# Optimization experiments

Hardware: AMD Instinct MI355X
Metric: run time of the kernel (lower is better)

The kernel has to match this reference:

```python
import jax, jax.numpy as jnp
import numpy as np

RMIN, RMAX = 10, 20
GAP = RMAX - RMIN          # 10
NUMR = GAP + 1             # 11
NSTEP = 64
BATCH = 8192
P = 128
HID = 64
MC = 10000
T_TOTAL = 1.0
DT = T_TOTAL / NSTEP
DXC = 0.5                  # D (x diffusion)
DYC = 0.5                  # Dy
RDOM = 5.0                 # reflecting sphere radius for xb
CAP_EPS = 0.1              # capture distance
F32 = jnp.float32


def _jump_size(uvals, ridx, jump_measure):
    # uvals: [M] uniforms, ridx: [M] int row index into [NUMR, 2*GAP] measure
    cnt = (uvals[:, None] < jump_measure[ridx]).sum(axis=1)
    ind = 2 * GAP - cnt
    return jnp.where(ind < GAP, ind + 1, -(ind - GAP + 1)).astype(jnp.int32)


def _forward(u, jump_r, jump_l, W1, b1, W2, b2, W3, b3, emb,
             Wf1, bf1, Wf2, bf2, Wf3, bf3,
             rt0, xt0, yt0, dBxt, dByt, jump_unif, size_unif, mc_unif,
             jump_measure, cr, cfr):
    fix_x = jnp.array([1.0, 0.0, 0.0], F32)
    G = jnp.array([[0.0, 0.0], [0.0, 1.0], [-1.0, 0.0]], F32)  # grad_eucl_polar

    # Monte-Carlo jump compensation: E[jump_l(jump_size(r))] * cr, per r level
    ridx_mc = jnp.tile(jnp.arange(NUMR, dtype=jnp.int32), MC)
    s = _jump_size(mc_unif, ridx_mc, jump_measure)
    a = jnp.abs(s) - 1
    mcj = jump_l[0][a] * (s > 0)[:, None] + jump_l[1][a] * (s < 0)[:, None]
    mc_jump = mcj.reshape(MC, NUMR, P).mean(axis=0) * cr  # [NUMR, P]

    eye = jnp.broadcast_to(jnp.eye(3, dtype=F32), (BATCH, 3, 3))
    carry0 = (rt0, xt0, xt0, yt0, eye, eye,
              jnp.ones((BATCH, 1), F32) * u,        # u_pre
              jnp.zeros((BATCH, 1), F32),           # fun
              jnp.ones((BATCH, 1), F32))            # run mask

    def reflect(pos, gt):
        nr = jnp.linalg.norm(pos, axis=1, keepdims=True)
        nb = pos / jnp.maximum(nr, 1e-12)
        out = nr[:, 0] > RDOM
        pos = jnp.where(out[:, None], nb * (2.0 * RDOM - nr), pos)
        proj = jnp.einsum('bi,bij->bj', nb, gt)
        gt = jnp.where(out[:, None, None], gt - 2.0 * nb[:, :, None] * proj[:, None, :], gt)
        return pos, gt

    def step(carry, xs):
        rt, xt, xt_in, yt_in, gtx, gty, u_pre, fun, run = carry
        dbx, dby, ju, su, w1, bb1, w2, bb2, w3, bb3, em, wf1, bff1, wf2, bff2, wf3, bff3 = xs
        ridx = jnp.clip(rt - RMIN, 0, GAP)
        jump_on = ju < cr[ridx, 0] * DT
        drt = _jump_size(su, ridx, jump_measure) * jump_on.astype(jnp.int32)
        # polar angles of xt (theta shifted by pi/2, as in forward)
        nx = jnp.maximum(jnp.linalg.norm(xt, axis=1), 1e-12)
        th = jnp.arccos(jnp.clip(xt[:, 2] / nx, -1.0, 1.0)) - jnp.pi / 2
        ph = jnp.arctan2(xt[:, 1], xt[:, 0])
        ct, st_, cp, sp = jnp.cos(th), jnp.sin(th), jnp.cos(ph), jnp.sin(ph)
        z = jnp.zeros_like(ct)
        # T_inv = Rz(phi) @ Ry(theta - pi/2), maps local frame at fix_x to xt
        T_inv = jnp.stack([jnp.stack([cp * ct, -sp, cp * st_], 1),
                           jnp.stack([sp * ct, cp, sp * st_], 1),
                           jnp.stack([-st_, z, ct], 1)], axis=1)  # [B,3,3]
        inp6 = jnp.concatenate([xt_in, yt_in], axis=1)  # [B,6]
        # TNN: low-rank net, r-embedding contracted with MLP output [B,P,6]
        h = jnp.tanh(inp6 @ w1 + bb1)
        h = jnp.tanh(h @ w2 + bb2)
        gu = jnp.einsum('bp,bpo->bo', em[ridx], (h @ w3 + bb3).reshape(BATCH, P, 6))
        v = jnp.einsum('bi,bij->bj', gu[:, :3], gtx)
        v = jnp.einsum('bi,bij->bj', v, T_inv)
        grad_ux = v @ G                                     # [B,2]
        grad_uy = jnp.einsum('bi,bij->bj', gu[:, 3:], gty)  # [B,3]
        aidx = jnp.clip(jnp.abs(drt) - 1, 0, GAP - 1)
        jl = jump_l[0][aidx] * (drt > 0)[:, None] + jump_l[1][aidx] * (drt < 0)[:, None]
        hf = jnp.tanh(inp6 @ wf1 + bff1)
        hf = jnp.tanh(hf @ wf2 + bff2)
        jx = hf @ wf3 + bff3                                 # FNN [B,P]
        jump = (jx * jump_r[ridx] * (jl - mc_jump[ridx] * DT)).sum(1, keepdims=True)
        rtf = rt.astype(F32)[:, None]
        sdx = jnp.sqrt(2.0 * DXC) / rtf
        diff = (sdx * (grad_ux * dbx).sum(1, keepdims=True)
                + jnp.sqrt(2.0 * DYC) * (grad_uy * dby).sum(1, keepdims=True) + jump)
        u_pre = u_pre + run * jnp.exp(-fun) * diff
        fun = fun + cfr[ridx] * DT
        # SDE update on the sphere (local angular increment rotated by T_inv)
        dX = sdx * dbx
        tht = dX[:, 0] + jnp.pi / 2
        pht = dX[:, 1]
        cart = jnp.stack([jnp.sin(tht) * jnp.cos(pht),
                          jnp.sin(tht) * jnp.sin(pht),
                          jnp.cos(tht)], 1) - fix_x
        dX3 = jnp.einsum('bij,bj->bi', T_inv, cart)
        xt = xt + dX3
        xt_in = xt_in + jnp.einsum('bij,bj->bi', gtx, dX3)
        yt_in = yt_in + jnp.sqrt(2.0 * DYC) * jnp.einsum('bij,bj->bi', gty, dby)
        rt = jnp.clip(rt + drt, RMIN, RMAX)
        xt_in, gtx = reflect(xt_in, gtx)
        yt_in, gty = reflect(yt_in, gty)
        cap = jnp.linalg.norm(xt_in - yt_in, axis=1, keepdims=True) < CAP_EPS
        run = run * jnp.where(cap, 0.0, 1.0)
        return (rt, xt, xt_in, yt_in, gtx, gty, u_pre, fun, run), None

    xs = (dBxt, dByt, jump_unif, size_unif, W1, b1, W2, b2, W3, b3, emb,
          Wf1, bf1, Wf2, bf2, Wf3, bf3)
    carry, _ = jax.lax.scan(step, carry0, xs)
    rt, xt, xt_in, yt_in, gtx, gty, u_pre, fun, run = carry
    u0v = jnp.exp(-jnp.sum((xt_in - yt_in) ** 2, axis=1, keepdims=True))
    u_rel = run * u0v * jnp.exp(-fun)
    return u_pre, u_rel


def setup_inputs() -> dict:
    key = jax.random.key(0)
    ks = jax.random.split(key, 24)

    def nrm(k, shape, fan):
        return jax.random.normal(k, shape, dtype=F32) / np.float32(np.sqrt(fan))

    # birth/death rate tables, forward equation: alpha(r,k)=mu(r+k,k), beta(r,k)=lamb(r-k,k)
    kk = np.arange(1, GAP + 1, dtype=np.float32)
    rr = np.arange(RMIN, RMAX + 1, dtype=np.float32)[:, None]
    lamb = 0.6 * rr / (kk * (kk + 1))
    mu = 0.5 * rr / (kk * (kk + 1))
    alpha = 0.5 * (rr + kk) / (kk * (kk + 1))
    beta = 0.6 * np.maximum(rr - kk, 0.0) / (kk * (kk + 1))
    jm = np.concatenate([alpha, beta], axis=1).cumsum(axis=1)
    cr = jm[:, -1:]
    jump_measure = jm / cr
    cfr = lamb.sum(1, keepdims=True) + mu.sum(1, keepdims=True) - cr

    x0 = jax.random.normal(ks[17], (BATCH, 3), dtype=F32)
    x0 = x0 / jnp.linalg.norm(x0, axis=1, keepdims=True)
    y0 = jax.random.normal(ks[18], (BATCH, 3), dtype=F32)

    return dict(
        u=jax.random.uniform(ks[0], (1,), dtype=F32),
        jump_r=nrm(ks[1], (NUMR, P), P),
        jump_l=nrm(ks[2], (2, GAP, P), P),
        W1=nrm(ks[3], (NSTEP, 6, HID), 6), b1=jnp.zeros((NSTEP, HID), F32),
        W2=nrm(ks[4], (NSTEP, HID, HID), HID), b2=jnp.zeros((NSTEP, HID), F32),
        W3=nrm(ks[5], (NSTEP, HID, P * 6), HID), b3=jnp.zeros((NSTEP, P * 6), F32),
        emb=nrm(ks[6], (NSTEP, NUMR, P), P),
        Wf1=nrm(ks[7], (NSTEP, 6, HID), 6), bf1=jnp.zeros((NSTEP, HID), F32),
        Wf2=nrm(ks[8], (NSTEP, HID, HID), HID), bf2=jnp.zeros((NSTEP, HID), F32),
        Wf3=nrm(ks[9], (NSTEP, HID, P), HID), bf3=jnp.zeros((NSTEP, P), F32),
        rt0=jax.random.randint(ks[10], (BATCH,), RMIN, RMAX + 1, dtype=jnp.int32),
        xt0=x0,
        yt0=y0,
        dBxt=jax.random.normal(ks[11], (NSTEP, BATCH, 2), dtype=F32) * np.float32(np.sqrt(DT)),
        dByt=jax.random.normal(ks[12], (NSTEP, BATCH, 3), dtype=F32) * np.float32(np.sqrt(DT)),
        jump_unif=jax.random.uniform(ks[13], (NSTEP, BATCH), dtype=F32),
        size_unif=jax.random.uniform(ks[14], (NSTEP, BATCH), dtype=F32),
        mc_unif=jax.random.uniform(ks[15], (MC * NUMR,), dtype=F32),
        jump_measure=jnp.asarray(jump_measure),
        cr=jnp.asarray(cr),
        cfr=jnp.asarray(cfr),
    )


def reference(u, jump_r, jump_l, W1, b1, W2, b2, W3, b3, emb,
              Wf1, bf1, Wf2, bf2, Wf3, bf3,
              rt0, xt0, yt0, dBxt, dByt, jump_unif, size_unif, mc_unif,
              jump_measure, cr, cfr):
    return _forward(u, jump_r, jump_l, W1, b1, W2, b2, W3, b3, emb,
                    Wf1, bf1, Wf2, bf2, Wf3, bf3,
                    rt0, xt0, yt0, dBxt, dByt, jump_unif, size_unif, mc_unif,
                    jump_measure, cr, cfr)
```

## Files before the change

kernel.cpp:

```cpp
#include <hip/hip_runtime.h>
#include <math.h>

#define NUMR 11
#define NSTEP 64
#define BATCH 8192
#define PDIM 128
#define MC 10000
#define DT (1.0f/64.0f)
#define RDOM 5.0f
#define CAP_EPS 0.1f
#define TP (NSTEP*BATCH)

#define OFF_HIST 0
#define OFF_W3EB 256
#define OFF_B3E  180480
#define OFF_BT   186112
#define OFF_BB   1087232
#define OFF_W2A  1101312
#define OFF_WF2A 1232384
#define OFF_GEO  1363456
#define OFF_SM   7654912
#define OFF_CONTRIB 8703488

typedef __attribute__((ext_vector_type(8))) short short8;
typedef __attribute__((ext_vector_type(4))) float f32x4;

__device__ __forceinline__ float tanh_f(float x) {
    float e = __expf(2.0f * x);
    return 1.0f - 2.0f * __builtin_amdgcn_rcpf(e + 1.0f);
}
__device__ __forceinline__ unsigned short bf16bits(float f) {
    unsigned u = __float_as_uint(f);
    return (unsigned short)((u + 0x7FFFu + ((u >> 16) & 1u)) >> 16);
}
__device__ __forceinline__ float bf16f(unsigned short s) {
    return __uint_as_float(((unsigned)s) << 16);
}
__device__ __forceinline__ unsigned cvt_pk_bf16(float lo, float hi) {
    unsigned r;
    asm("v_cvt_pk_bf16_f32 %0, %1, %2" : "=v"(r) : "v"(lo), "v"(hi));
    return r;
}

__device__ __forceinline__ void reflect3(float* p, float* g) {
    float nr = sqrtf(p[0]*p[0] + p[1]*p[1] + p[2]*p[2]);
    if (nr > RDOM) {
        float inv = 1.0f / fmaxf(nr, 1e-12f);
        float nb0 = p[0]*inv, nb1 = p[1]*inv, nb2 = p[2]*inv;
        float sc = 2.0f*RDOM - nr;
        p[0] = nb0*sc; p[1] = nb1*sc; p[2] = nb2*sc;
        #pragma unroll
        for (int j = 0; j < 3; ++j) {
            float proj = nb0*g[j] + nb1*g[3+j] + nb2*g[6+j];
            g[j]   -= 2.0f*nb0*proj;
            g[3+j] -= 2.0f*nb1*proj;
            g[6+j] -= 2.0f*nb2*proj;
        }
    }
}

__launch_bounds__(256)
__global__ void k_prep(const int* __restrict__ rt0, const float* __restrict__ xt0,
                       const float* __restrict__ yt0, const float* __restrict__ dBx,
                       const float* __restrict__ dBy, const float* __restrict__ junif,
                       const float* __restrict__ sunif, const float* __restrict__ jm,
                       const float* __restrict__ cr, const float* __restrict__ cfr,
                       const float* __restrict__ mcu,
                       const float* __restrict__ W2, const float* __restrict__ Wf2,
                       const float* __restrict__ W3, const float* __restrict__ b3,
                       const float* __restrict__ emb, const float* __restrict__ Wf3,
                       const float* __restrict__ bf3, const float* __restrict__ jump_r,
                       const float* __restrict__ jump_l,
                       float* ws, int* hist, float* out) {
    __shared__ float smem[6440];
    int blk = blockIdx.x, tid = threadIdx.x;

    if (blk < 128) {
        float* sjm = smem; float* scr = smem + 220; float* smul = smem + 231;
        for (int i = tid; i < 220; i += 256) sjm[i] = jm[i];
        if (tid < 11) { scr[tid] = cr[tid]; smul[tid] = __expf(-cfr[tid]*DT); }
        __syncthreads();
        if (tid >= 64) return;
        int p = blk * 64 + tid;

        int rt = rt0[p];
        float xt[3], xin[3], yin[3], gtx[9], gty[9];
        #pragma unroll
        for (int i = 0; i < 3; ++i) { xt[i] = xt0[p*3+i]; xin[i] = xt[i]; yin[i] = yt0[p*3+i]; }
        #pragma unroll
        for (int i = 0; i < 9; ++i) { gtx[i] = (i % 4 == 0) ? 1.f : 0.f; gty[i] = gtx[i]; }
        float ef = 1.f, run = 1.f;

        float ju = junif[p], su = sunif[p];
        float dbx0 = dBx[(size_t)p*2], dbx1 = dBx[(size_t)p*2+1];
        float dby0 = dBy[(size_t)p*3], dby1 = dBy[(size_t)p*3+1], dby2 = dBy[(size_t)p*3+2];

        float* GEO = ws + OFF_GEO;
        float* SM  = ws + OFF_SM;
        #pragma unroll 1
        for (int t = 0; t < NSTEP; ++t) {
            float nju=0.f,nsu=0.f,ndbx0=0.f,ndbx1=0.f,ndby0=0.f,ndby1=0.f,ndby2=0.f;
            if (t < NSTEP-1) {
                int nb = (t+1)*BATCH + p;
                nju = junif[nb]; nsu = sunif[nb];
                ndbx0 = dBx[(size_t)nb*2]; ndbx1 = dBx[(size_t)nb*2+1];
                ndby0 = dBy[(size_t)nb*3]; ndby1 = dBy[(size_t)nb*3+1]; ndby2 = dBy[(size_t)nb*3+2];
            }
            int base = t*BATCH + p;
            int r = rt - 10;
            int jon = (ju < scr[r]*DT) ? 1 : 0;
            int cnt = 0;
            #pragma unroll
            for (int j = 0; j < 20; ++j) cnt += (su < sjm[r*20+j]) ? 1 : 0;
            int ind = 20 - cnt;
            int drt = (ind < 10) ? (ind+1) : -(ind-9);
            drt = jon ? drt : 0;
            int sa = (drt > 0) ? (drt-1) : ((drt < 0) ? (9-drt) : 0);
            int jf = (drt != 0) ? 1 : 0;

            float nx = fmaxf(sqrtf(xt[0]*xt[0]+xt[1]*xt[1]+xt[2]*xt[2]), 1e-12f);
            float c = fminf(1.f, fmaxf(-1.f, xt[2]/nx));
            float ct = sqrtf(fmaxf(0.f, 1.f - c*c));
            float st = -c;
            float rxy2 = xt[0]*xt[0] + xt[1]*xt[1];
            float cp = 1.f, sp = 0.f;
            if (rxy2 > 0.f) { float ir = 1.0f/sqrtf(rxy2); cp = xt[0]*ir; sp = xt[1]*ir; }
            float Ti[9];
            Ti[0]=cp*ct; Ti[1]=-sp; Ti[2]=cp*st;
            Ti[3]=sp*ct; Ti[4]=cp;  Ti[5]=sp*st;
            Ti[6]=-st;   Ti[7]=0.f; Ti[8]=ct;

            float sdx = 1.0f/(float)(r+10);
            float scale = run * ef;

            float cx[3], cy[3];
            #pragma unroll
            for (int i = 0; i < 3; ++i) {
                float w31 = gtx[i*3]*Ti[1] + gtx[i*3+1]*Ti[4] + gtx[i*3+2]*Ti[7];
                float w32 = gtx[i*3]*Ti[2] + gtx[i*3+1]*Ti[5] + gtx[i*3+2]*Ti[8];
                cx[i] = sdx * (w31*dbx1 - w32*dbx0);
                cy[i] = gty[i*3]*dby0 + gty[i*3+1]*dby1 + gty[i*3+2]*dby2;
            }
            float* gp = GEO + (size_t)base*12;
            float4 v0 = {xin[0], xin[1], xin[2], yin[0]};
            float4 v1 = {yin[1], yin[2], cx[0], cx[1]};
            float4 v2 = {cx[2], cy[0], cy[1], cy[2]};
            *(float4*)(gp)     = v0;
            *(float4*)(gp + 4) = v1;
            *(float4*)(gp + 8) = v2;
            float2 smv = {scale, __int_as_float(r | (sa<<8) | (jf<<16))};
            *(float2*)(SM + (size_t)base*2) = smv;

            ef *= smul[r];

            float dX0 = sdx*dbx0, dX1 = sdx*dbx1;
            float x2 = dX0*dX0, y2 = dX1*dX1;
            float s0 = dX0*(1.f - x2*(1.f/6.f));
            float cc0 = 1.f - x2*0.5f + x2*x2*(1.f/24.f);
            float s1 = dX1*(1.f - y2*(1.f/6.f));
            float cc1 = 1.f - y2*0.5f + y2*y2*(1.f/24.f);
            float cart0 = cc0*cc1 - 1.0f, cart1 = cc0*s1, cart2 = -s0;
            float dX3[3];
            #pragma unroll
            for (int i = 0; i < 3; ++i)
                dX3[i] = Ti[i*3]*cart0 + Ti[i*3+1]*cart1 + Ti[i*3+2]*cart2;
            #pragma unroll
            for (int i = 0; i < 3; ++i) xt[i] += dX3[i];
            #pragma unroll
            for (int i = 0; i < 3; ++i)
                xin[i] += gtx[i*3]*dX3[0] + gtx[i*3+1]*dX3[1] + gtx[i*3+2]*dX3[2];
            #pragma unroll
            for (int i = 0; i < 3; ++i)
                yin[i] += gty[i*3]*dby0 + gty[i*3+1]*dby1 + gty[i*3+2]*dby2;
            rt += drt; rt = (rt < 10) ? 10 : ((rt > 20) ? 20 : rt);
            reflect3(xin, gtx);
            reflect3(yin, gty);
            float d0 = xin[0]-yin[0], d1 = xin[1]-yin[1], d2 = xin[2]-yin[2];
            if (sqrtf(d0*d0 + d1*d1 + d2*d2) < CAP_EPS) run = 0.f;

            ju = nju; su = nsu; dbx0 = ndbx0; dbx1 = ndbx1;
            dby0 = ndby0; dby1 = ndby1; dby2 = ndby2;
        }
        float d0 = xin[0]-yin[0], d1 = xin[1]-yin[1], d2 = xin[2]-yin[2];
        float u0v = __expf(-(d0*d0 + d1*d1 + d2*d2));
        out[BATCH + p] = run * u0v * ef;

    } else if (blk < 236) {
        int* lh = (int*)smem;
        for (int i = tid; i < 220; i += 256) lh[i] = 0;
        __syncthreads();
        int hb = blk - 128;
        #pragma unroll
        for (int j = 0; j < 4; ++j) {
            int i = hb*1024 + j*256 + tid;
            if (i < MC*NUMR) {
                int r = i % NUMR;
                float u = mcu[i];
                int cnt = 0;
                #pragma unroll
                for (int k = 0; k < 20; ++k) cnt += (u < jm[r*20+k]) ? 1 : 0;
                int ind = 20 - cnt;
                int s = (ind < 10) ? (ind+1) : -(ind-9);
                int sa = (s > 0) ? (s-1) : (10 + (-s-1));
                atomicAdd(&lh[r*20+sa], 1);
            }
        }
        __syncthreads();
        if (tid < 220 && lh[tid]) atomicAdd(&hist[tid], lh[tid]);

    } else if (blk < 300) {
        int t = blk - 236;
        unsigned short* W2A  = (unsigned short*)(ws + OFF_W2A)  + t*4096;
        unsigned short* WF2A = (unsigned short*)(ws + OFF_WF2A) + t*4096;
        for (int i = tid; i < 4096; i += 256) {
            int j = i & 7, L = (i >> 3) & 63, ktct = i >> 9;
            int ct = ktct >> 1, kt = ktct & 1;
            int c = ct*16 + (L & 15);
            int k = kt*32 + (L >> 4)*8 + j;
            W2A[i]  = bf16bits(W2[t*4096 + k*64 + c]);
            WF2A[i] = bf16bits(Wf2[t*4096 + k*64 + c]);
        }

    } else {
        int idx = blk - 300;
        int t = idx / 65, kk = idx % 65;
        bool brow = (kk == 64);
        const float* w3row = brow ? (b3 + t*768) : (W3 + (t*64+kk)*768);
        const float* wfrow = brow ? (bf3 + t*128) : (Wf3 + (t*64+kk)*128);
        unsigned short* W3EB = (unsigned short*)(ws + OFF_W3EB);

        float* sW3  = smem;
        float* sWf  = smem + 768;
        float* sEmb = smem + 896;
        float* sJr  = smem + 2348;
        float* sJl  = smem + 3800;
        for (int i = tid; i < 768; i += 256) sW3[i] = w3row[i];
        if (tid < 128) sWf[tid] = wfrow[tid];
        for (int i = tid; i < 1408; i += 256) {
            int r = i >> 7, p = i & 127;
            sEmb[r*132 + p] = emb[(t*11+r)*128 + p];
            sJr[r*132 + p]  = jump_r[i];
        }
        for (int i = tid; i < 2560; i += 256) {
            int sa = i >> 7, p = i & 127;
            sJl[sa*132 + p] = jump_l[i];
        }
        __syncthreads();

        for (int q = tid; q < 286; q += 256) {
            if (q < 66) {
                int o = q / 11, r = q % 11;
                const float* e = sEmb + r*132;
                float a0 = 0.f, a1 = 0.f;
                #pragma unroll 4
                for (int p = 0; p < 128; p += 2) {
                    a0 = fmaf(e[p],   sW3[p*6+o],     a0);
                    a1 = fmaf(e[p+1], sW3[(p+1)*6+o], a1);
                }
                float acc = a0 + a1;
                if (brow) ws[OFF_B3E + (t*11+r)*8 + o] = acc;
                else      W3EB[(size_t)((t*11+r)*64 + kk)*8 + o] = bf16bits(acc);
            } else {
                int qq = q - 66;
                int sa = qq / 11, r = qq % 11;
                const float* jr = sJr + r*132;
                const float* jl = sJl + sa*132;
                float a0 = 0.f, a1 = 0.f;
                #pragma unroll 4
                for (int p = 0; p < 128; p += 2) {
                    a0 = fmaf(sWf[p],   jr[p]   * jl[p],   a0);
                    a1 = fmaf(sWf[p+1], jr[p+1] * jl[p+1], a1);
                }
                float acc = a0 + a1;
                if (brow) ws[OFF_BB + (t*11+r)*20 + sa] = acc;
                else      ws[OFF_BT + ((size_t)(t*11+r)*20 + sa)*64 + kk] = acc;
            }
        }
    }
}

__global__ void k_fold(const int* __restrict__ hist, const float* __restrict__ cr,
                       float* ws) {
    int t = blockIdx.x, tid = threadIdx.x;
    unsigned short* W3EB = (unsigned short*)(ws + OFF_W3EB);
    for (int i = tid; i < 715; i += 256) {
        if (i < 704) {
            int r = i >> 6, c = i & 63;
            float crn = cr[r] * (1.0f/(float)MC);
            const float* btp = ws + OFF_BT + (size_t)(t*11+r)*20*64 + c;
            float acc = 0.f;
            #pragma unroll
            for (int sa = 0; sa < 20; ++sa)
                acc += (float)hist[r*20+sa] * btp[sa*64];
            W3EB[(size_t)((t*11+r)*64 + c)*8 + 6] = bf16bits(acc * crn * (-DT));
        } else {
            int r = i - 704;
            float crn = cr[r] * (1.0f/(float)MC);
            float acc = 0.f;
            #pragma unroll
            for (int sa = 0; sa < 20; ++sa)
                acc += (float)hist[r*20+sa] * ws[OFF_BB + (t*11+r)*20 + sa];
            ws[OFF_B3E + (t*11+r)*8 + 6] = acc * crn * (-DT);
        }
    }
}

__launch_bounds__(256, 4)
__global__ void k_mlp(const float* __restrict__ ws,
                      const float* __restrict__ W1, const float* __restrict__ b1,
                      const float* __restrict__ Wf1, const float* __restrict__ bf1,
                      const float* __restrict__ b2, const float* __restrict__ bf2,
                      float* __restrict__ contrib) {
    __shared__ unsigned short sW2[4096], sWf2[4096];
    __shared__ unsigned short sW3E[11*520];
    __shared__ float sB3E[11*12];
    __shared__ float sBB[220];
    int tid = threadIdx.x;
    int t = blockIdx.x & 63;
    {
        const unsigned* g2  = (const unsigned*)((const unsigned short*)(ws + OFF_W2A)  + t*4096);
        const unsigned* g2f = (const unsigned*)((const unsigned short*)(ws + OFF_WF2A) + t*4096);
        unsigned* s2  = (unsigned*)sW2;
        unsigned* s2f = (unsigned*)sWf2;
        #pragma unroll
        for (int i = 0; i < 8; ++i) {
            s2[i*256 + tid]  = g2[i*256 + tid];
            s2f[i*256 + tid] = g2f[i*256 + tid];
        }
        const unsigned* g3 = (const unsigned*)((const unsigned short*)(ws + OFF_W3EB) + (size_t)t*5632);
        unsigned* s3 = (unsigned*)sW3E;
        for (int i = tid; i < 2816; i += 256) {
            int r = i >> 8, off = i & 255;
            s3[r*260 + off] = g3[i];
        }
        if (tid < 88) {
            int r = tid >> 3, o = tid & 7;
            sB3E[r*12 + o] = ws[OFF_B3E + t*88 + tid];
        }
        if (tid < 220) sBB[tid] = ws[OFF_BB + t*220 + tid];
    }
    __syncthreads();
    int L = tid & 63, l15 = L & 15, q4 = L >> 4;
    int pbase = (blockIdx.x >> 6) * 256 + (tid >> 6) * 64;

    float4 bh4[4], bf4[4];
    #pragma unroll
    for (int ct = 0; ct < 4; ++ct) {
        bh4[ct] = *(const float4*)(b2  + t*64 + ct*16 + q4*4);
        bf4[ct] = *(const float4*)(bf2 + t*64 + ct*16 + q4*4);
    }
    const float* GEO = ws + OFF_GEO;
    const float* SM  = ws + OFF_SM;
    const float* W1t  = W1  + t*384;
    const float* Wf1t = Wf1 + t*384;
    const float* b1t  = b1  + t*64;
    const float* bf1t = bf1 + t*64;

    int base_n = t*BATCH + pbase + l15;
    float2 sm_n = *(const float2*)(SM + (size_t)base_n*2);
    float4 ga_n = *(const float4*)(GEO + (size_t)base_n*12);
    float4 gb_n = *(const float4*)(GEO + (size_t)base_n*12 + 4);
    float4 gc_n = *(const float4*)(GEO + (size_t)base_n*12 + 8);

    #pragma unroll 1
    for (int g = 0; g < 4; ++g) {
        int base = base_n;
        float2 sm = sm_n;
        float4 ga = ga_n, gb = gb_n, gc = gc_n;
        if (g < 3) {
            base_n = t*BATCH + pbase + (g+1)*16 + l15;
            sm_n = *(const float2*)(SM + (size_t)base_n*2);
            ga_n = *(const float4*)(GEO + (size_t)base_n*12);
            gb_n = *(const float4*)(GEO + (size_t)base_n*12 + 4);
            gc_n = *(const float4*)(GEO + (size_t)base_n*12 + 8);
        }
        float scale = sm.x;
        if (__ballot(scale != 0.f) == 0ULL) {
            if (q4 == 0) contrib[base] = 0.f;
            continue;
        }
        int meta = __float_as_int(sm.y);
        float inp[6]  = {ga.x, ga.y, ga.z, ga.w, gb.x, gb.y};
        float coef[6] = {gb.z, gb.w, gc.x, gc.y, gc.z, gc.w};
        int r = meta & 255, sa = (meta >> 8) & 255;
        bool jump = ((meta >> 16) & 1) != 0;

        short8 bh[2], bfr[2];
        #pragma unroll
        for (int kt = 0; kt < 2; ++kt) {
            int kb = kt*32 + q4*8;
            float av[8], fv[8];
            #pragma unroll
            for (int j = 0; j < 8; ++j) { av[j] = b1t[kb+j]; fv[j] = bf1t[kb+j]; }
            #pragma unroll
            for (int i = 0; i < 6; ++i) {
                float x = inp[i];
                #pragma unroll
                for (int j = 0; j < 8; ++j) {
                    av[j] = fmaf(x, W1t[i*64 + kb + j],  av[j]);
                    fv[j] = fmaf(x, Wf1t[i*64 + kb + j], fv[j]);
                }
            }
            short8 vh, vf;
            unsigned* vhp = (unsigned*)&vh;
            unsigned* vfp = (unsigned*)&vf;
            #pragma unroll
            for (int j = 0; j < 4; ++j) {
                vhp[j] = cvt_pk_bf16(tanh_f(av[2*j]), tanh_f(av[2*j+1]));
                vfp[j] = cvt_pk_bf16(tanh_f(fv[2*j]), tanh_f(fv[2*j+1]));
            }
            bh[kt] = vh; bfr[kt] = vf;
        }

        const unsigned short* W3E8 = sW3E + r*520;
        const float* btp = ws + OFF_BT + ((size_t)(t*11 + r)*20 + sa)*64;
        float pdp = 0.f;
        #pragma unroll
        for (int ct = 0; ct < 4; ++ct) {
            short8 a0 = *(const short8*)(sW2  + ((ct*2 + 0)*64 + L)*8);
            short8 a1 = *(const short8*)(sW2  + ((ct*2 + 1)*64 + L)*8);
            short8 c0 = *(const short8*)(sWf2 + ((ct*2 + 0)*64 + L)*8);
            short8 c1 = *(const short8*)(sWf2 + ((ct*2 + 1)*64 + L)*8);
            f32x4 acc  = {bh4[ct].x, bh4[ct].y, bh4[ct].z, bh4[ct].w};
            f32x4 accf = {bf4[ct].x, bf4[ct].y, bf4[ct].z, bf4[ct].w};
            acc  = __builtin_amdgcn_mfma_f32_16x16x32_bf16(a0, bh[0],  acc,  0, 0, 0);
            acc  = __builtin_amdgcn_mfma_f32_16x16x32_bf16(a1, bh[1],  acc,  0, 0, 0);
            accf = __builtin_amdgcn_mfma_f32_16x16x32_bf16(c0, bfr[0], accf, 0, 0, 0);
            accf = __builtin_amdgcn_mfma_f32_16x16x32_bf16(c1, bfr[1], accf, 0, 0, 0);
            #pragma unroll
            for (int reg = 0; reg < 4; ++reg) {
                float h2 = tanh_f(acc[reg]);
                float f2 = tanh_f(accf[reg]);
                int c = ct*16 + q4*4 + reg;
                short8 wv = *(const short8*)(W3E8 + c*8);
                float s = bf16f((unsigned short)wv[0])*coef[0]
                        + bf16f((unsigned short)wv[1])*coef[1]
                        + bf16f((unsigned short)wv[2])*coef[2]
                        + bf16f((unsigned short)wv[3])*coef[3]
                        + bf16f((unsigned short)wv[4])*coef[4]
                        + bf16f((unsigned short)wv[5])*coef[5];
                pdp = fmaf(h2, s, pdp);
                pdp = fmaf(f2, bf16f((unsigned short)wv[6]), pdp);
                if (jump) pdp = fmaf(f2, btp[c], pdp);
            }
        }
        pdp += __shfl_xor(pdp, 16, 64);
        pdp += __shfl_xor(pdp, 32, 64);

        const float* B3E8 = sB3E + r*12;
        float4 ba  = *(const float4*)(B3E8);
        float4 bbv = *(const float4*)(B3E8 + 4);
        float dpart = pdp
            + ba.x*coef[0] + ba.y*coef[1] + ba.z*coef[2]
            + ba.w*coef[3] + bbv.x*coef[4] + bbv.y*coef[5]
            + bbv.z;
        if (jump) dpart += sBB[r*20 + sa];
        if (q4 == 0) contrib[base] = scale * dpart;
    }
}

__global__ void k_reduce(const float* __restrict__ contrib, const float* __restrict__ u,
                         float* out) {
    __shared__ float red[256];
    int tid = threadIdx.x;
    int pi = tid & 31, tc = tid >> 5;
    int p = blockIdx.x * 32 + pi;
    float a = 0.f;
    #pragma unroll
    for (int j = 0; j < 8; ++j) a += contrib[(tc*8 + j)*BATCH + p];
    red[tid] = a;
    __syncthreads();
    if (tid < 32) {
        float s = u[0];
        #pragma unroll
        for (int c = 0; c < 8; ++c) s += red[c*32 + pi];
        out[p] = s;
    }
}

extern "C" void kernel_launch(void* const* d_in, const int* in_sizes, int n_in,
                              void* d_out, int out_size, void* d_ws, size_t ws_size,
                              hipStream_t stream) {
    const float* u      = (const float*)d_in[0];
    const float* jump_r = (const float*)d_in[1];
    const float* jump_l = (const float*)d_in[2];
    const float* W1  = (const float*)d_in[3];
    const float* b1  = (const float*)d_in[4];
    const float* W2  = (const float*)d_in[5];
    const float* b2  = (const float*)d_in[6];
    const float* W3  = (const float*)d_in[7];
    const float* b3  = (const float*)d_in[8];
    const float* emb = (const float*)d_in[9];
    const float* Wf1 = (const float*)d_in[10];
    const float* bf1 = (const float*)d_in[11];
    const float* Wf2 = (const float*)d_in[12];
    const float* bf2 = (const float*)d_in[13];
    const float* Wf3 = (const float*)d_in[14];
    const float* bf3 = (const float*)d_in[15];
    const int*   rt0 = (const int*)d_in[16];
    const float* xt0 = (const float*)d_in[17];
    const float* yt0 = (const float*)d_in[18];
    const float* dBx = (const float*)d_in[19];
    const float* dBy = (const float*)d_in[20];
    const float* junif = (const float*)d_in[21];
    const float* sunif = (const float*)d_in[22];
    const float* mcu = (const float*)d_in[23];
    const float* jm  = (const float*)d_in[24];
    const float* cr  = (const float*)d_in[25];
    const float* cfr = (const float*)d_in[26];
    float* ws  = (float*)d_ws;
    float* out = (float*)d_out;

    hipMemsetAsync(ws + OFF_HIST, 0, 220*sizeof(int), stream);
    k_prep<<<4460, 256, 0, stream>>>(rt0, xt0, yt0, dBx, dBy, junif, sunif,
                                     jm, cr, cfr, mcu, W2, Wf2,
                                     W3, b3, emb, Wf3, bf3, jump_r, jump_l,
                                     ws, (int*)(ws + OFF_HIST), out);
    k_fold<<<64, 256, 0, stream>>>((const int*)(ws + OFF_HIST), cr, ws);
    k_mlp<<<2048, 256, 0, stream>>>(ws, W1, b1, Wf1, bf1, b2, bf2,
                                    ws + OFF_CONTRIB);
    k_reduce<<<256, 256, 0, stream>>>(ws + OFF_CONTRIB, u, out);
}
```

Before: 292.5 us.

## Fuse histogram fold into MLP kernel and replace reduction with atomics

Removes the separate fold kernel by having each MLP block compute the MC-histogram-weighted jump compensation terms directly into shared memory. It also drops the contrib buffer and the reduce kernel: out is initialised to u in the prep kernel and each block atomically adds its per-path contributions. This cuts two launches and a global round trip. In exchange, every one of the 2048 blocks redoes the fold work for its time step, and float atomics on the output make the summation order nondeterministic.

```diff
diff --git a/kernel.cpp b/kernel.cpp
--- a/kernel.cpp
+++ b/kernel.cpp
@@ -20,7 +20,6 @@
 #define OFF_WF2A 1232384
 #define OFF_GEO  1363456
 #define OFF_SM   7654912
-#define OFF_CONTRIB 8703488
 
 typedef __attribute__((ext_vector_type(8))) short short8;
 typedef __attribute__((ext_vector_type(4))) float f32x4;
@@ -70,7 +69,7 @@
                        const float* __restrict__ W3, const float* __restrict__ b3,
                        const float* __restrict__ emb, const float* __restrict__ Wf3,
                        const float* __restrict__ bf3, const float* __restrict__ jump_r,
-                       const float* __restrict__ jump_l,
+                       const float* __restrict__ jump_l, const float* __restrict__ u,
                        float* ws, int* hist, float* out) {
     __shared__ float smem[6440];
     int blk = blockIdx.x, tid = threadIdx.x;
@@ -186,6 +185,8 @@
         out[BATCH + p] = run * u0v * ef;
 
     } else if (blk < 236) {
+        int gp = (blk - 128) * 256 + tid;
+        if (gp < BATCH) out[gp] = u[0];
         int* lh = (int*)smem;
         for (int i = tid; i < 220; i += 256) lh[i] = 0;
         __syncthreads();
@@ -195,10 +196,10 @@
             int i = hb*1024 + j*256 + tid;
             if (i < MC*NUMR) {
                 int r = i % NUMR;
-                float u = mcu[i];
+                float uu = mcu[i];
                 int cnt = 0;
                 #pragma unroll
-                for (int k = 0; k < 20; ++k) cnt += (u < jm[r*20+k]) ? 1 : 0;
+                for (int k = 0; k < 20; ++k) cnt += (uu < jm[r*20+k]) ? 1 : 0;
                 int ind = 20 - cnt;
                 int s = (ind < 10) ? (ind+1) : -(ind-9);
                 int sa = (s > 0) ? (s-1) : (10 + (-s-1));
@@ -279,38 +280,13 @@
     }
 }
 
-__global__ void k_fold(const int* __restrict__ hist, const float* __restrict__ cr,
-                       float* ws) {
-    int t = blockIdx.x, tid = threadIdx.x;
-    unsigned short* W3EB = (unsigned short*)(ws + OFF_W3EB);
-    for (int i = tid; i < 715; i += 256) {
-        if (i < 704) {
-            int r = i >> 6, c = i & 63;
-            float crn = cr[r] * (1.0f/(float)MC);
-            const float* btp = ws + OFF_BT + (size_t)(t*11+r)*20*64 + c;
-            float acc = 0.f;
-            #pragma unroll
-            for (int sa = 0; sa < 20; ++sa)
-                acc += (float)hist[r*20+sa] * btp[sa*64];
-            W3EB[(size_t)((t*11+r)*64 + c)*8 + 6] = bf16bits(acc * crn * (-DT));
-        } else {
-            int r = i - 704;
-            float crn = cr[r] * (1.0f/(float)MC);
-            float acc = 0.f;
-            #pragma unroll
-            for (int sa = 0; sa < 20; ++sa)
-                acc += (float)hist[r*20+sa] * ws[OFF_BB + (t*11+r)*20 + sa];
-            ws[OFF_B3E + (t*11+r)*8 + 6] = acc * crn * (-DT);
-        }
-    }
-}
-
 __launch_bounds__(256, 4)
 __global__ void k_mlp(const float* __restrict__ ws,
                       const float* __restrict__ W1, const float* __restrict__ b1,
                       const float* __restrict__ Wf1, const float* __restrict__ bf1,
                       const float* __restrict__ b2, const float* __restrict__ bf2,
-                      float* __restrict__ contrib) {
+                      const int* __restrict__ hist, const float* __restrict__ cr,
+                      float* __restrict__ out) {
     __shared__ unsigned short sW2[4096], sWf2[4096];
     __shared__ unsigned short sW3E[11*520];
     __shared__ float sB3E[11*12];
@@ -340,6 +316,28 @@
         if (tid < 220) sBB[tid] = ws[OFF_BB + t*220 + tid];
     }
     __syncthreads();
+    for (int i = tid; i < 715; i += 256) {
+        if (i < 704) {
+            int r = i >> 6, c = i & 63;
+            float crn = cr[r] * (1.0f/(float)MC);
+            const float* btp = ws + OFF_BT + (size_t)(t*11+r)*20*64 + c;
+            float acc = 0.f;
+            #pragma unroll
+            for (int sa = 0; sa < 20; ++sa)
+                acc += (float)hist[r*20+sa] * btp[sa*64];
+            sW3E[r*520 + c*8 + 6] = bf16bits(acc * crn * (-DT));
+        } else {
+            int r = i - 704;
+            float crn = cr[r] * (1.0f/(float)MC);
+            float acc = 0.f;
+            #pragma unroll
+            for (int sa = 0; sa < 20; ++sa)
+                acc += (float)hist[r*20+sa] * sBB[r*20+sa];
+            sB3E[r*12 + 6] = acc * crn * (-DT);
+        }
+    }
+    __syncthreads();
+
     int L = tid & 63, l15 = L & 15, q4 = L >> 4;
     int pbase = (blockIdx.x >> 6) * 256 + (tid >> 6) * 64;
 
@@ -375,10 +373,7 @@
             gc_n = *(const float4*)(GEO + (size_t)base_n*12 + 8);
         }
         float scale = sm.x;
-        if (__ballot(scale != 0.f) == 0ULL) {
-            if (q4 == 0) contrib[base] = 0.f;
-            continue;
-        }
+        if (__ballot(scale != 0.f) == 0ULL) continue;
         int meta = __float_as_int(sm.y);
         float inp[6]  = {ga.x, ga.y, ga.z, ga.w, gb.x, gb.y};
         float coef[6] = {gb.z, gb.w, gc.x, gc.y, gc.z, gc.w};
@@ -455,26 +450,10 @@
             + ba.w*coef[3] + bbv.x*coef[4] + bbv.y*coef[5]
             + bbv.z;
         if (jump) dpart += sBB[r*20 + sa];
-        if (q4 == 0) contrib[base] = scale * dpart;
-    }
-}
-
-__global__ void k_reduce(const float* __restrict__ contrib, const float* __restrict__ u,
-                         float* out) {
-    __shared__ float red[256];
-    int tid = threadIdx.x;
-    int pi = tid & 31, tc = tid >> 5;
-    int p = blockIdx.x * 32 + pi;
-    float a = 0.f;
-    #pragma unroll
-    for (int j = 0; j < 8; ++j) a += contrib[(tc*8 + j)*BATCH + p];
-    red[tid] = a;
-    __syncthreads();
-    if (tid < 32) {
-        float s = u[0];
-        #pragma unroll
-        for (int c = 0; c < 8; ++c) s += red[c*32 + pi];
-        out[p] = s;
+        if (q4 == 0) {
+            int pidx = base - t*BATCH;
+            atomicAdd(&out[pidx], scale * dpart);
+        }
     }
 }
 
@@ -514,10 +493,8 @@
     hipMemsetAsync(ws + OFF_HIST, 0, 220*sizeof(int), stream);
     k_prep<<<4460, 256, 0, stream>>>(rt0, xt0, yt0, dBx, dBy, junif, sunif,
                                      jm, cr, cfr, mcu, W2, Wf2,
-                                     W3, b3, emb, Wf3, bf3, jump_r, jump_l,
+                                     W3, b3, emb, Wf3, bf3, jump_r, jump_l, u,
                                      ws, (int*)(ws + OFF_HIST), out);
-    k_fold<<<64, 256, 0, stream>>>((const int*)(ws + OFF_HIST), cr, ws);
     k_mlp<<<2048, 256, 0, stream>>>(ws, W1, b1, Wf1, bf1, b2, bf2,
-                                    ws + OFF_CONTRIB);
-    k_reduce<<<256, 256, 0, stream>>>(ws + OFF_CONTRIB, u, out);
-}
+                                    (const int*)(ws + OFF_HIST), cr, out);
+}
```

Result: slower. 299.5 us (+2.4%).
